# Kernel optimization log

Hardware: AMD Instinct MI355X
Metric: run time of the kernel (lower is better)

Reference implementation:

```python
import jax, jax.numpy as jnp
import numpy as np

STEPS = 10          # points in t_grid -> STEPS-1 RK4 intervals
TRACE_STEPS = 2     # Hutchinson probes per dynamics eval
T_FINAL = 1.0
CLAMP = 100.0


def odefun(t, z, W1, b1, tw1, W2, b2):
    # time-conditioned 2-layer tanh MLP (canonical FFJORD dynamics)
    h = jnp.tanh(z @ W1 + b1 + t * tw1)
    return h @ W2 + b2


def setup_inputs() -> dict:
    key = jax.random.key(0)
    B, D, H = 2048, 512, 1024
    ks = jax.random.split(key, 4)
    s1 = 1.0 / np.sqrt(D)
    s2 = 1.0 / np.sqrt(H)
    return {
        "x": jax.random.normal(ks[0], (B, D), jnp.float32),
        "W1": jax.random.normal(ks[1], (D, H), jnp.float32) * s1,
        "b1": jnp.zeros((H,), jnp.float32),
        "tw1": jax.random.normal(ks[2], (H,), jnp.float32) * 0.1,
        "W2": jax.random.normal(ks[3], (H, D), jnp.float32) * s2,
        "b2": jnp.zeros((D,), jnp.float32),
    }


def reference(x, W1, b1, tw1, W2, b2):
    params = (W1, b1, tw1, W2, b2)
    B, D = x.shape

    def divergence_estimate(t, z, e):
        # torch detaches z before the grad call -> stop_gradient here
        z_sg = jax.lax.stop_gradient(z)
        f, vjp_fn = jax.vjp(lambda zz: odefun(t, zz, *params), z_sg)
        etf = vjp_fn(e)[0]                      # e^T J  (Hutchinson probe)
        return f, jnp.sum(etf * e, axis=-1)     # [B]

    def augmented_dynamics(t, state, key):
        z = state[:, :-1]                        # [B, D]
        div_est = jnp.zeros((B,), state.dtype)
        f_z = None
        for i in range(TRACE_STEPS):             # small fixed loop
            e = jax.random.randint(jax.random.fold_in(key, i), z.shape, 0, 2).astype(z.dtype) * 2.0 - 1.0
            f_z, div = divergence_estimate(t, z, e)
            div_est = div_est + div
        div_est = jnp.clip(div_est / TRACE_STEPS, -CLAMP, CLAMP)
        return jnp.concatenate([f_z, -div_est[:, None]], axis=-1)

    t_grid = jnp.linspace(0.0, T_FINAL, STEPS)
    state0 = jnp.concatenate([x, jnp.zeros((B, 1), x.dtype)], axis=-1)  # [B, D+1]

    def step(carry, t01):
        state, key = carry
        t0, t1 = t01[0], t01[1]
        dt = t1 - t0
        key, k1k, k2k, k3k, k4k = jax.random.split(key, 5)
        # torchdiffeq 'rk4' = Kutta's 3/8-rule variant (rk4_alt_step_func)
        k1 = augmented_dynamics(t0, state, k1k)
        k2 = augmented_dynamics(t0 + dt / 3.0, state + dt * k1 / 3.0, k2k)
        k3 = augmented_dynamics(t0 + dt * 2.0 / 3.0, state + dt * (k2 - k1 / 3.0), k3k)
        k4 = augmented_dynamics(t1, state + dt * (k1 - k2 + k3), k4k)
        state = state + (k1 + 3.0 * (k2 + k3) + k4) * dt * 0.125
        return (state, key), None

    t_pairs = jnp.stack([t_grid[:-1], t_grid[1:]], axis=-1)  # [STEPS-1, 2]
    (state, _), _ = jax.lax.scan(step, (state0, jax.random.key(1234)), t_pairs)

    rep, probsolve = state[:, :-1], state[:, -1]
    logprob = -0.5 * jnp.sum(rep * rep, axis=-1) + probsolve
    return rep, logprob
```

## Files before the change

kernel.cpp:

```cpp
#include <hip/hip_runtime.h>
#include <stdint.h>


#define B_N 2048
#define D_N 512
#define H_N 1024
#define BD (B_N * D_N)

typedef unsigned short u16;
typedef __attribute__((ext_vector_type(8))) short s16x8;
typedef __attribute__((ext_vector_type(4))) float f32x4;

typedef __attribute__((address_space(1))) const uint32_t ga_u32;
typedef __attribute__((address_space(3))) uint32_t ls_u32;

#if __has_builtin(__builtin_amdgcn_alignbit)
#define ROTL32(x, r) __builtin_amdgcn_alignbit((x), (x), 32 - (r))
#else
#define ROTL32(x, r) (((x) << (r)) | ((x) >> (32 - (r))))
#endif

__device__ __forceinline__ float bf2f(u16 u) {
  union { uint32_t u; float f; } c; c.u = ((uint32_t)u) << 16; return c.f;
}
__device__ __forceinline__ u16 f2bf(float f) {
  union { float f; uint32_t u; } c; c.f = f;
  uint32_t r = c.u + 0x7FFFu + ((c.u >> 16) & 1u);
  return (u16)(r >> 16);
}

struct U2 { uint32_t x, y; };

__device__ __forceinline__ U2 tf2x32(uint32_t k0, uint32_t k1, uint32_t x0, uint32_t x1) {
  uint32_t k2 = k0 ^ k1 ^ 0x1BD11BDAu;
#define RND(r) { x0 += x1; x1 = ROTL32(x1, r); x1 ^= x0; }
  x0 += k0; x1 += k1;
  RND(13) RND(15) RND(26) RND(6)
  x0 += k1; x1 += k2 + 1u;
  RND(17) RND(29) RND(16) RND(24)
  x0 += k2; x1 += k0 + 2u;
  RND(13) RND(15) RND(26) RND(6)
  x0 += k0; x1 += k1 + 3u;
  RND(17) RND(29) RND(16) RND(24)
  x0 += k1; x1 += k2 + 4u;
  RND(13) RND(15) RND(26) RND(6)
  x0 += k2; x1 += k0 + 5u;
#undef RND
  U2 r; r.x = x0; r.y = x1; return r;
}

__global__ void k_keysched(uint32_t* __restrict__ ekeys) {
  if (threadIdx.x != 0 || blockIdx.x != 0) return;
  uint32_t kx = 0u, ky = 1234u;
  for (int s = 0; s < 9; ++s) {
    for (int st = 0; st < 4; ++st) {
      U2 kst = tf2x32(kx, ky, 0u, (uint32_t)(st + 1));
      for (int pr = 0; pr < 2; ++pr) {
        U2 fo = tf2x32(kst.x, kst.y, 0u, (uint32_t)pr);
        U2 k2 = tf2x32(fo.x, fo.y, 0u, 1u);
        ekeys[(s * 4 + st) * 4 + pr * 2 + 0] = k2.x;
        ekeys[(s * 4 + st) * 4 + pr * 2 + 1] = k2.y;
      }
    }
    U2 c = tf2x32(kx, ky, 0u, 0u);
    kx = c.x; ky = c.y;
  }
}

__global__ void k_egen(u16* __restrict__ ebf, const uint32_t* __restrict__ keys, int gs) {
  int t = blockIdx.x * 256 + threadIdx.x;
  int stage = gs + (t >> 16), rem = t & 65535;
  int probe = rem >> 15, idx = rem & 32767;
  uint32_t p0 = (uint32_t)idx * 32;
  uint32_t k0 = keys[stage * 4 + probe * 2], k1 = keys[stage * 4 + probe * 2 + 1];
  uint4* dst = (uint4*)(ebf + (size_t)(stage & 3) * (2 * (size_t)BD) + (size_t)probe * BD + (size_t)idx * 32);
#pragma unroll
  for (int g = 0; g < 4; ++g) {
    uint32_t pr[4];
#pragma unroll
    for (int h = 0; h < 4; ++h) {
      uint32_t c0 = p0 + g * 8 + h * 2;
      U2 r0 = tf2x32(k0, k1, 0u, c0);
      U2 r1 = tf2x32(k0, k1, 0u, c0 + 1u);
      pr[h] = (((r0.x ^ r0.y) & 1u) ? 0x3F80u : 0xBF80u) |
              (((r1.x ^ r1.y) & 1u) ? 0x3F800000u : 0xBF800000u);
    }
    uint4 v; v.x = pr[0]; v.y = pr[1]; v.z = pr[2]; v.w = pr[3];
    dst[g] = v;
  }
}

__global__ void k_init(const float* __restrict__ x, float* __restrict__ z, u16* __restrict__ zin,
                       float* __restrict__ lp, float* __restrict__ d0, float* __restrict__ d1) {
  int i = blockIdx.x * 256 + threadIdx.x;
  if (i < BD) { float v = x[i]; z[i] = v; zin[i] = f2bf(v); }
  if (i < B_N) { lp[i] = 0.f; d0[i] = 0.f; d1[i] = 0.f; }
}

__global__ void k_cvtT(const float* __restrict__ src, u16* __restrict__ dst, int R, int C) {
  int i = blockIdx.x * 256 + threadIdx.x;
  if (i >= R * C) return;
  int c = i / R, r = i - c * R;
  dst[i] = f2bf(src[(size_t)r * C + c]);
}
__global__ void k_cvt(const float* __restrict__ src, u16* __restrict__ dst, int n) {
  int i = blockIdx.x * 256 + threadIdx.x;
  if (i < n) dst[i] = f2bf(src[i]);
}

__global__ void k_sentinel(float* __restrict__ out, int n) {
  int i = blockIdx.x * 256 + threadIdx.x;
  if (i < n) out[i] = 12345.0f;
}

__global__ __launch_bounds__(256)
void k_f1(const u16* __restrict__ zin, const u16* __restrict__ e0g, const u16* __restrict__ e1g,
          const u16* __restrict__ W1T, const u16* __restrict__ W2b,
          const float* __restrict__ b1, const float* __restrict__ tw1, float tstage,
          u16* __restrict__ hbuf, float* __restrict__ div0, float* __restrict__ div1) {
  __shared__ u16 S[2][5 * 2048];
  const int tid = threadIdx.x, wave = tid >> 6, lane = tid & 63;
  const int bm = blockIdx.x >> 4;
  const int bh = blockIdx.x & 15;
  const int row0 = bm * 64, col0 = bh * 64;
  const int wm = wave >> 1, wn = wave & 1, r16 = lane & 15, q = lane >> 4;
  const int srow = lane >> 2, scol = (lane & 3) * 8;

  f32x4 az[2][2], au0[2][2], au1[2][2], av0[2][2], av1[2][2];
#pragma unroll
  for (int i = 0; i < 2; ++i)
#pragma unroll
    for (int j = 0; j < 2; ++j) {
      az[i][j] = (f32x4){0,0,0,0}; au0[i][j] = (f32x4){0,0,0,0}; au1[i][j] = (f32x4){0,0,0,0};
      av0[i][j] = (f32x4){0,0,0,0}; av1[i][j] = (f32x4){0,0,0,0};
    }

  const size_t arow = (size_t)(row0 + wave * 16 + srow) * 512 + scol;
  const size_t brow = (size_t)(col0 + wave * 16 + srow) * 512 + scol;
  auto stage = [&](int kt, int buf) {
    u16* b = &S[buf][0];
    __builtin_amdgcn_global_load_lds((ga_u32*)(zin + arow + kt), (ls_u32*)(b + 0    + wave * 512), 16, 0, 0);
    __builtin_amdgcn_global_load_lds((ga_u32*)(e0g + arow + kt), (ls_u32*)(b + 2048 + wave * 512), 16, 0, 0);
    __builtin_amdgcn_global_load_lds((ga_u32*)(e1g + arow + kt), (ls_u32*)(b + 4096 + wave * 512), 16, 0, 0);
    __builtin_amdgcn_global_load_lds((ga_u32*)(W1T + brow + kt), (ls_u32*)(b + 6144 + wave * 512), 16, 0, 0);
    __builtin_amdgcn_global_load_lds((ga_u32*)(W2b + brow + kt), (ls_u32*)(b + 8192 + wave * 512), 16, 0, 0);
  };
  stage(0, 0);
  for (int it = 0; it < 16; ++it) {
    const int buf = it & 1;
    __syncthreads();
    if (it + 1 < 16) stage((it + 1) * 32, buf ^ 1);
    const u16* b = &S[buf][0];
    s16x8 zf[2], e0f[2], e1f[2], w1f[2], w2f[2];
#pragma unroll
    for (int i = 0; i < 2; ++i) {
      const int ao = (wm * 32 + i * 16 + r16) * 32 + q * 8;
      zf[i]  = *(const s16x8*)(b + 0    + ao);
      e0f[i] = *(const s16x8*)(b + 2048 + ao);
      e1f[i] = *(const s16x8*)(b + 4096 + ao);
    }
#pragma unroll
    for (int j = 0; j < 2; ++j) {
      const int bo = (wn * 32 + j * 16 + r16) * 32 + q * 8;
      w1f[j] = *(const s16x8*)(b + 6144 + bo);
      w2f[j] = *(const s16x8*)(b + 8192 + bo);
    }
#pragma unroll
    for (int i = 0; i < 2; ++i)
#pragma unroll
      for (int j = 0; j < 2; ++j) {
        az[i][j]  = __builtin_amdgcn_mfma_f32_16x16x32_bf16(zf[i],  w1f[j], az[i][j],  0, 0, 0);
        au0[i][j] = __builtin_amdgcn_mfma_f32_16x16x32_bf16(e0f[i], w1f[j], au0[i][j], 0, 0, 0);
        au1[i][j] = __builtin_amdgcn_mfma_f32_16x16x32_bf16(e1f[i], w1f[j], au1[i][j], 0, 0, 0);
        av0[i][j] = __builtin_amdgcn_mfma_f32_16x16x32_bf16(e0f[i], w2f[j], av0[i][j], 0, 0, 0);
        av1[i][j] = __builtin_amdgcn_mfma_f32_16x16x32_bf16(e1f[i], w2f[j], av1[i][j], 0, 0, 0);
      }
  }

  float d0s[2][4], d1s[2][4];
#pragma unroll
  for (int i = 0; i < 2; ++i)
#pragma unroll
    for (int r = 0; r < 4; ++r) { d0s[i][r] = 0.f; d1s[i][r] = 0.f; }

#pragma unroll
  for (int j = 0; j < 2; ++j) {
    const int gcol = col0 + wn * 32 + j * 16 + r16;
    const float colb = b1[gcol] + tstage * tw1[gcol];
#pragma unroll
    for (int i = 0; i < 2; ++i) {
      const int rbase = row0 + wm * 32 + i * 16 + q * 4;
#pragma unroll
      for (int r = 0; r < 4; ++r) {
        float hv = tanhf(az[i][j][r] + colb);
        hbuf[(size_t)(rbase + r) * H_N + gcol] = f2bf(hv);
        float s = 1.f - hv * hv;
        d0s[i][r] += s * au0[i][j][r] * av0[i][j][r];
        d1s[i][r] += s * au1[i][j][r] * av1[i][j][r];
      }
    }
  }
#pragma unroll
  for (int i = 0; i < 2; ++i)
#pragma unroll
    for (int r = 0; r < 4; ++r) {
      float a = d0s[i][r], b = d1s[i][r];
#pragma unroll
      for (int m = 1; m < 16; m <<= 1) { a += __shfl_xor(a, m); b += __shfl_xor(b, m); }
      if (r16 == 0) {
        int grow = row0 + wm * 32 + i * 16 + q * 4 + r;
        atomicAdd(&div0[grow], a);
        atomicAdd(&div1[grow], b);
      }
    }
}

template<int ST>
__global__ __launch_bounds__(256)
void k_f3(const u16* __restrict__ hbuf, const u16* __restrict__ W2T, const float* __restrict__ b2,
          float* __restrict__ z, float* __restrict__ ACC, float* __restrict__ T,
          u16* __restrict__ zin, float dt,
          float* __restrict__ lp, float* __restrict__ div0, float* __restrict__ div1, float wdt) {
  __shared__ u16 S[2][2 * 2048];
  const int tid = threadIdx.x, wave = tid >> 6, lane = tid & 63;
  const int bm = blockIdx.x >> 3;
  const int bn = blockIdx.x & 7;
  const int row0 = bm * 64, col0 = bn * 64;
  const int wm = wave >> 1, wn = wave & 1, r16 = lane & 15, q = lane >> 4;
  const int srow = lane >> 2, scol = (lane & 3) * 8;

  if (bn == 0 && tid < 64) {
    int b = row0 + tid;
    float c = 0.5f * (div0[b] + div1[b]);
    c = fminf(fmaxf(c, -100.f), 100.f);
    lp[b] -= wdt * c;
    div0[b] = 0.f; div1[b] = 0.f;
  }

  f32x4 acc[2][2];
#pragma unroll
  for (int i = 0; i < 2; ++i)
#pragma unroll
    for (int j = 0; j < 2; ++j) acc[i][j] = (f32x4){0,0,0,0};

  const size_t arow = (size_t)(row0 + wave * 16 + srow) * 1024 + scol;
  const size_t brow = (size_t)(col0 + wave * 16 + srow) * 1024 + scol;
  auto stage = [&](int kt, int buf) {
    u16* b = &S[buf][0];
    __builtin_amdgcn_global_load_lds((ga_u32*)(hbuf + arow + kt), (ls_u32*)(b + 0    + wave * 512), 16, 0, 0);
    __builtin_amdgcn_global_load_lds((ga_u32*)(W2T  + brow + kt), (ls_u32*)(b + 2048 + wave * 512), 16, 0, 0);
  };
  stage(0, 0);
  for (int it = 0; it < 32; ++it) {
    const int buf = it & 1;
    __syncthreads();
    if (it + 1 < 32) stage((it + 1) * 32, buf ^ 1);
    const u16* b = &S[buf][0];
    s16x8 af[2], bfr[2];
#pragma unroll
    for (int i = 0; i < 2; ++i)
      af[i] = *(const s16x8*)(b + (wm * 32 + i * 16 + r16) * 32 + q * 8);
#pragma unroll
    for (int j = 0; j < 2; ++j)
      bfr[j] = *(const s16x8*)(b + 2048 + (wn * 32 + j * 16 + r16) * 32 + q * 8);
#pragma unroll
    for (int i = 0; i < 2; ++i)
#pragma unroll
      for (int j = 0; j < 2; ++j)
        acc[i][j] = __builtin_amdgcn_mfma_f32_16x16x32_bf16(af[i], bfr[j], acc[i][j], 0, 0, 0);
  }

#pragma unroll
  for (int j = 0; j < 2; ++j) {
    const int gcol = col0 + wn * 32 + j * 16 + r16;
    const float cb = b2[gcol];
#pragma unroll
    for (int i = 0; i < 2; ++i) {
      const int rbase = row0 + wm * 32 + i * 16 + q * 4;
#pragma unroll
      for (int r = 0; r < 4; ++r) {
        const size_t idx = (size_t)(rbase + r) * D_N + gcol;
        const float f = acc[i][j][r] + cb;
        if (ST == 0) {
          ACC[idx] = dt * 0.125f * f;
          T[idx]   = dt * f;
          zin[idx] = f2bf(z[idx] + dt * f * (1.f / 3.f));
        } else if (ST == 1) {
          float t_ = T[idx];
          ACC[idx] += 0.375f * dt * f;
          zin[idx] = f2bf(z[idx] + dt * f - t_ * (1.f / 3.f));
          T[idx]   = t_ - dt * f;
        } else if (ST == 2) {
          ACC[idx] += 0.375f * dt * f;
          zin[idx] = f2bf(z[idx] + T[idx] + dt * f);
        } else {
          float zn = z[idx] + ACC[idx] + dt * 0.125f * f;
          z[idx]   = zn;
          zin[idx] = f2bf(zn);
        }
      }
    }
  }
}

__global__ void k_out(const float* __restrict__ z, const float* __restrict__ lp,
                      float* __restrict__ out) {
  int b = blockIdx.x, t = threadIdx.x;
  const float* zr = z + (size_t)b * D_N;
  float ss = 0.f;
  for (int d = t; d < D_N; d += 256) {
    float v = zr[d];
    out[(size_t)b * D_N + d] = v;
    ss += v * v;
  }
  for (int off = 32; off > 0; off >>= 1) ss += __shfl_down(ss, off);
  __shared__ float red[4];
  if ((t & 63) == 0) red[t >> 6] = ss;
  __syncthreads();
  if (t == 0) out[(size_t)BD + b] = -0.5f * (red[0] + red[1] + red[2] + red[3]) + lp[b];
}

extern "C" void kernel_launch(void* const* d_in, const int* in_sizes, int n_in,
                              void* d_out, int out_size, void* d_ws, size_t ws_size,
                              hipStream_t stream) {
  const float* x   = (const float*)d_in[0];
  const float* W1  = (const float*)d_in[1];
  const float* b1  = (const float*)d_in[2];
  const float* tw1 = (const float*)d_in[3];
  const float* W2  = (const float*)d_in[4];
  const float* b2  = (const float*)d_in[5];

  const size_t NEEDED = (size_t)45 << 20;
  if (ws_size < NEEDED) {
    k_sentinel<<<(BD + B_N + 255) / 256, 256, 0, stream>>>((float*)d_out, BD + B_N);
    return;
  }
  char* w = (char*)d_ws;
  auto carve = [&](size_t bytes) { char* p = w; w += (bytes + 255) & ~(size_t)255; return p; };
  uint32_t* keys = (uint32_t*)carve(144 * sizeof(uint32_t));
  u16* ebf   = (u16*)carve((size_t)4 * 2 * BD * 2);
  float* z   = (float*)carve((size_t)BD * 4);
  float* ACC = (float*)carve((size_t)BD * 4);
  float* T   = (float*)carve((size_t)BD * 4);
  u16* zin   = (u16*)carve((size_t)BD * 2);
  u16* hbuf  = (u16*)carve((size_t)B_N * H_N * 2);
  u16* W1T   = (u16*)carve((size_t)H_N * D_N * 2);
  u16* W2b   = (u16*)carve((size_t)H_N * D_N * 2);
  u16* W2T   = (u16*)carve((size_t)D_N * H_N * 2);
  float* lp   = (float*)carve((size_t)B_N * 4);
  float* div0 = (float*)carve((size_t)B_N * 4);
  float* div1 = (float*)carve((size_t)B_N * 4);

  k_keysched<<<1, 1, 0, stream>>>(keys);
  k_init<<<BD / 256, 256, 0, stream>>>(x, z, zin, lp, div0, div1);
  k_cvtT<<<(D_N * H_N) / 256, 256, 0, stream>>>(W1, W1T, D_N, H_N);
  k_cvt <<<(H_N * D_N) / 256, 256, 0, stream>>>(W2, W2b, H_N * D_N);
  k_cvtT<<<(H_N * D_N) / 256, 256, 0, stream>>>(W2, W2T, H_N, D_N);

  const int gF1 = (B_N / 64) * (H_N / 64);
  const int gF3 = (B_N / 64) * (D_N / 64);

  for (int s = 0; s < 9; ++s) {
    float t0 = (float)s / 9.0f;
    float t1 = (float)(s + 1) / 9.0f;
    float dt = t1 - t0;
    float tst[4] = { t0, t0 + dt / 3.0f, t0 + dt * 2.0f / 3.0f, t1 };
    float wts[4] = { 1.f, 3.f, 3.f, 1.f };
    for (int st = 0; st < 4; ++st) {
      const int sg = s * 4 + st;
      if ((sg & 3) == 0) k_egen<<<1024, 256, 0, stream>>>(ebf, keys, sg);
      const u16* e0g = ebf + (size_t)(sg & 3) * (2 * (size_t)BD);
      const u16* e1g = e0g + BD;
      k_f1<<<gF1, 256, 0, stream>>>(zin, e0g, e1g, W1T, W2b, b1, tw1, tst[st], hbuf, div0, div1);
      const float wdt = dt * 0.125f * wts[st];
      if (st == 0)      k_f3<0><<<gF3, 256, 0, stream>>>(hbuf, W2T, b2, z, ACC, T, zin, dt, lp, div0, div1, wdt);
      else if (st == 1) k_f3<1><<<gF3, 256, 0, stream>>>(hbuf, W2T, b2, z, ACC, T, zin, dt, lp, div0, div1, wdt);
      else if (st == 2) k_f3<2><<<gF3, 256, 0, stream>>>(hbuf, W2T, b2, z, ACC, T, zin, dt, lp, div0, div1, wdt);
      else              k_f3<3><<<gF3, 256, 0, stream>>>(hbuf, W2T, b2, z, ACC, T, zin, dt, lp, div0, div1, wdt);
    }
  }
  k_out<<<B_N, 256, 0, stream>>>(z, lp, (float*)d_out);
}
```

Baseline: 1.476 ms.

## Fuse whole ODE solve into one persistent cooperative kernel with grid syncs

Replaces the per-stage launches of the f1/f3 GEMM kernels with a single cooperative persistent kernel that loops over all 36 RK stages, separated by grid-wide syncs, and folds init, weight conversion and output into it. All Rademacher probes are precomputed up front into a much larger buffer (36 stages instead of 4). The f3 tile is also shrunk to 64x32 so there are 512 tiles, evenly spread across the persistent blocks. This removes launch gaps, at the cost of a larger workspace requirement, grid-sync overhead, and lower per-wave MFMA reuse in f3.

```diff
diff --git a/kernel.cpp b/kernel.cpp
--- a/kernel.cpp
+++ b/kernel.cpp
@@ -1,4 +1,5 @@
 #include <hip/hip_runtime.h>
+#include <hip/hip_cooperative_groups.h>
 #include <stdint.h>
 
 
@@ -6,6 +7,8 @@
 #define D_N 512
 #define H_N 1024
 #define BD (B_N * D_N)
+
+namespace cg = cooperative_groups;
 
 typedef unsigned short u16;
 typedef __attribute__((ext_vector_type(8))) short s16x8;
@@ -20,9 +23,6 @@
 #define ROTL32(x, r) (((x) << (r)) | ((x) >> (32 - (r))))
 #endif
 
-__device__ __forceinline__ float bf2f(u16 u) {
-  union { uint32_t u; float f; } c; c.u = ((uint32_t)u) << 16; return c.f;
-}
 __device__ __forceinline__ u16 f2bf(float f) {
   union { float f; uint32_t u; } c; c.f = f;
   uint32_t r = c.u + 0x7FFFu + ((c.u >> 16) & 1u);
@@ -49,8 +49,7 @@
   U2 r; r.x = x0; r.y = x1; return r;
 }
 
-__global__ void k_keysched(uint32_t* __restrict__ ekeys) {
-  if (threadIdx.x != 0 || blockIdx.x != 0) return;
+__device__ __forceinline__ void keysched_body(uint32_t* ekeys) {
   uint32_t kx = 0u, ky = 1234u;
   for (int s = 0; s < 9; ++s) {
     for (int st = 0; st < 4; ++st) {
@@ -67,13 +66,13 @@
   }
 }
 
-__global__ void k_egen(u16* __restrict__ ebf, const uint32_t* __restrict__ keys, int gs) {
-  int t = blockIdx.x * 256 + threadIdx.x;
-  int stage = gs + (t >> 16), rem = t & 65535;
+__device__ __forceinline__ void egen_item(int t2, u16* __restrict__ ebf,
+                                          const uint32_t* __restrict__ keys) {
+  int stage = t2 >> 16, rem = t2 & 65535;
   int probe = rem >> 15, idx = rem & 32767;
   uint32_t p0 = (uint32_t)idx * 32;
   uint32_t k0 = keys[stage * 4 + probe * 2], k1 = keys[stage * 4 + probe * 2 + 1];
-  uint4* dst = (uint4*)(ebf + (size_t)(stage & 3) * (2 * (size_t)BD) + (size_t)probe * BD + (size_t)idx * 32);
+  uint4* dst = (uint4*)(ebf + (size_t)stage * (2 * (size_t)BD) + (size_t)probe * BD + (size_t)idx * 32);
 #pragma unroll
   for (int g = 0; g < 4; ++g) {
     uint32_t pr[4];
@@ -90,38 +89,13 @@
   }
 }
 
-__global__ void k_init(const float* __restrict__ x, float* __restrict__ z, u16* __restrict__ zin,
-                       float* __restrict__ lp, float* __restrict__ d0, float* __restrict__ d1) {
-  int i = blockIdx.x * 256 + threadIdx.x;
-  if (i < BD) { float v = x[i]; z[i] = v; zin[i] = f2bf(v); }
-  if (i < B_N) { lp[i] = 0.f; d0[i] = 0.f; d1[i] = 0.f; }
-}
-
-__global__ void k_cvtT(const float* __restrict__ src, u16* __restrict__ dst, int R, int C) {
-  int i = blockIdx.x * 256 + threadIdx.x;
-  if (i >= R * C) return;
-  int c = i / R, r = i - c * R;
-  dst[i] = f2bf(src[(size_t)r * C + c]);
-}
-__global__ void k_cvt(const float* __restrict__ src, u16* __restrict__ dst, int n) {
-  int i = blockIdx.x * 256 + threadIdx.x;
-  if (i < n) dst[i] = f2bf(src[i]);
-}
-
-__global__ void k_sentinel(float* __restrict__ out, int n) {
-  int i = blockIdx.x * 256 + threadIdx.x;
-  if (i < n) out[i] = 12345.0f;
-}
-
-__global__ __launch_bounds__(256)
-void k_f1(const u16* __restrict__ zin, const u16* __restrict__ e0g, const u16* __restrict__ e1g,
-          const u16* __restrict__ W1T, const u16* __restrict__ W2b,
-          const float* __restrict__ b1, const float* __restrict__ tw1, float tstage,
-          u16* __restrict__ hbuf, float* __restrict__ div0, float* __restrict__ div1) {
-  __shared__ u16 S[2][5 * 2048];
+__device__ __forceinline__ void f1_tile(u16* S, int tile,
+    const u16* __restrict__ zin, const u16* __restrict__ e0g, const u16* __restrict__ e1g,
+    const u16* __restrict__ W1T, const u16* __restrict__ W2b,
+    const float* __restrict__ b1v, const float* __restrict__ tw1v, float tstage,
+    u16* __restrict__ hbuf, float* __restrict__ div0, float* __restrict__ div1) {
   const int tid = threadIdx.x, wave = tid >> 6, lane = tid & 63;
-  const int bm = blockIdx.x >> 4;
-  const int bh = blockIdx.x & 15;
+  const int bm = tile >> 4, bh = tile & 15;
   const int row0 = bm * 64, col0 = bh * 64;
   const int wm = wave >> 1, wn = wave & 1, r16 = lane & 15, q = lane >> 4;
   const int srow = lane >> 2, scol = (lane & 3) * 8;
@@ -138,7 +112,7 @@
   const size_t arow = (size_t)(row0 + wave * 16 + srow) * 512 + scol;
   const size_t brow = (size_t)(col0 + wave * 16 + srow) * 512 + scol;
   auto stage = [&](int kt, int buf) {
-    u16* b = &S[buf][0];
+    u16* b = S + buf * 10240;
     __builtin_amdgcn_global_load_lds((ga_u32*)(zin + arow + kt), (ls_u32*)(b + 0    + wave * 512), 16, 0, 0);
     __builtin_amdgcn_global_load_lds((ga_u32*)(e0g + arow + kt), (ls_u32*)(b + 2048 + wave * 512), 16, 0, 0);
     __builtin_amdgcn_global_load_lds((ga_u32*)(e1g + arow + kt), (ls_u32*)(b + 4096 + wave * 512), 16, 0, 0);
@@ -150,7 +124,7 @@
     const int buf = it & 1;
     __syncthreads();
     if (it + 1 < 16) stage((it + 1) * 32, buf ^ 1);
-    const u16* b = &S[buf][0];
+    const u16* b = S + buf * 10240;
     s16x8 zf[2], e0f[2], e1f[2], w1f[2], w2f[2];
 #pragma unroll
     for (int i = 0; i < 2; ++i) {
@@ -186,7 +160,7 @@
 #pragma unroll
   for (int j = 0; j < 2; ++j) {
     const int gcol = col0 + wn * 32 + j * 16 + r16;
-    const float colb = b1[gcol] + tstage * tw1[gcol];
+    const float colb = b1v[gcol] + tstage * tw1v[gcol];
 #pragma unroll
     for (int i = 0; i < 2; ++i) {
       const int rbase = row0 + wm * 32 + i * 16 + q * 4;
@@ -204,29 +178,26 @@
   for (int i = 0; i < 2; ++i)
 #pragma unroll
     for (int r = 0; r < 4; ++r) {
-      float a = d0s[i][r], b = d1s[i][r];
-#pragma unroll
-      for (int m = 1; m < 16; m <<= 1) { a += __shfl_xor(a, m); b += __shfl_xor(b, m); }
+      float a = d0s[i][r], bb = d1s[i][r];
+#pragma unroll
+      for (int m = 1; m < 16; m <<= 1) { a += __shfl_xor(a, m); bb += __shfl_xor(bb, m); }
       if (r16 == 0) {
         int grow = row0 + wm * 32 + i * 16 + q * 4 + r;
         atomicAdd(&div0[grow], a);
-        atomicAdd(&div1[grow], b);
+        atomicAdd(&div1[grow], bb);
       }
     }
 }
 
-template<int ST>
-__global__ __launch_bounds__(256)
-void k_f3(const u16* __restrict__ hbuf, const u16* __restrict__ W2T, const float* __restrict__ b2,
-          float* __restrict__ z, float* __restrict__ ACC, float* __restrict__ T,
-          u16* __restrict__ zin, float dt,
-          float* __restrict__ lp, float* __restrict__ div0, float* __restrict__ div1, float wdt) {
-  __shared__ u16 S[2][2 * 2048];
+__device__ __forceinline__ void f3_tile(u16* S, int tile,
+    const u16* __restrict__ hbuf, const u16* __restrict__ W2T, const float* __restrict__ b2v,
+    float* __restrict__ z, float* __restrict__ ACC, float* __restrict__ T,
+    u16* __restrict__ zin, float dt, int st,
+    float* __restrict__ lp, float* __restrict__ div0, float* __restrict__ div1, float wdt) {
   const int tid = threadIdx.x, wave = tid >> 6, lane = tid & 63;
-  const int bm = blockIdx.x >> 3;
-  const int bn = blockIdx.x & 7;
-  const int row0 = bm * 64, col0 = bn * 64;
-  const int wm = wave >> 1, wn = wave & 1, r16 = lane & 15, q = lane >> 4;
+  const int bm = tile >> 4, bn = tile & 15;
+  const int row0 = bm * 64, col0 = bn * 32;
+  const int r16 = lane & 15, q = lane >> 4;
   const int srow = lane >> 2, scol = (lane & 3) * 8;
 
   if (bn == 0 && tid < 64) {
@@ -237,72 +208,167 @@
     div0[b] = 0.f; div1[b] = 0.f;
   }
 
-  f32x4 acc[2][2];
-#pragma unroll
-  for (int i = 0; i < 2; ++i)
-#pragma unroll
-    for (int j = 0; j < 2; ++j) acc[i][j] = (f32x4){0,0,0,0};
+  f32x4 acc[2];
+  acc[0] = (f32x4){0,0,0,0}; acc[1] = (f32x4){0,0,0,0};
 
   const size_t arow = (size_t)(row0 + wave * 16 + srow) * 1024 + scol;
-  const size_t brow = (size_t)(col0 + wave * 16 + srow) * 1024 + scol;
+  const size_t brow = (size_t)(col0 + (wave & 1) * 16 + srow) * 1024 + scol;
   auto stage = [&](int kt, int buf) {
-    u16* b = &S[buf][0];
-    __builtin_amdgcn_global_load_lds((ga_u32*)(hbuf + arow + kt), (ls_u32*)(b + 0    + wave * 512), 16, 0, 0);
-    __builtin_amdgcn_global_load_lds((ga_u32*)(W2T  + brow + kt), (ls_u32*)(b + 2048 + wave * 512), 16, 0, 0);
+    u16* b = S + buf * 10240;
+    __builtin_amdgcn_global_load_lds((ga_u32*)(hbuf + arow + kt), (ls_u32*)(b + wave * 512), 16, 0, 0);
+    if (wave < 2)
+      __builtin_amdgcn_global_load_lds((ga_u32*)(W2T + brow + kt), (ls_u32*)(b + 2048 + wave * 512), 16, 0, 0);
   };
   stage(0, 0);
   for (int it = 0; it < 32; ++it) {
     const int buf = it & 1;
     __syncthreads();
     if (it + 1 < 32) stage((it + 1) * 32, buf ^ 1);
-    const u16* b = &S[buf][0];
-    s16x8 af[2], bfr[2];
-#pragma unroll
-    for (int i = 0; i < 2; ++i)
-      af[i] = *(const s16x8*)(b + (wm * 32 + i * 16 + r16) * 32 + q * 8);
-#pragma unroll
-    for (int j = 0; j < 2; ++j)
-      bfr[j] = *(const s16x8*)(b + 2048 + (wn * 32 + j * 16 + r16) * 32 + q * 8);
-#pragma unroll
-    for (int i = 0; i < 2; ++i)
-#pragma unroll
-      for (int j = 0; j < 2; ++j)
-        acc[i][j] = __builtin_amdgcn_mfma_f32_16x16x32_bf16(af[i], bfr[j], acc[i][j], 0, 0, 0);
+    const u16* b = S + buf * 10240;
+    s16x8 af  = *(const s16x8*)(b + (wave * 16 + r16) * 32 + q * 8);
+    s16x8 bf0 = *(const s16x8*)(b + 2048 + r16 * 32 + q * 8);
+    s16x8 bf1 = *(const s16x8*)(b + 2048 + (16 + r16) * 32 + q * 8);
+    acc[0] = __builtin_amdgcn_mfma_f32_16x16x32_bf16(af, bf0, acc[0], 0, 0, 0);
+    acc[1] = __builtin_amdgcn_mfma_f32_16x16x32_bf16(af, bf1, acc[1], 0, 0, 0);
   }
 
 #pragma unroll
   for (int j = 0; j < 2; ++j) {
-    const int gcol = col0 + wn * 32 + j * 16 + r16;
-    const float cb = b2[gcol];
-#pragma unroll
-    for (int i = 0; i < 2; ++i) {
-      const int rbase = row0 + wm * 32 + i * 16 + q * 4;
-#pragma unroll
-      for (int r = 0; r < 4; ++r) {
-        const size_t idx = (size_t)(rbase + r) * D_N + gcol;
-        const float f = acc[i][j][r] + cb;
-        if (ST == 0) {
-          ACC[idx] = dt * 0.125f * f;
-          T[idx]   = dt * f;
-          zin[idx] = f2bf(z[idx] + dt * f * (1.f / 3.f));
-        } else if (ST == 1) {
-          float t_ = T[idx];
-          ACC[idx] += 0.375f * dt * f;
-          zin[idx] = f2bf(z[idx] + dt * f - t_ * (1.f / 3.f));
-          T[idx]   = t_ - dt * f;
-        } else if (ST == 2) {
-          ACC[idx] += 0.375f * dt * f;
-          zin[idx] = f2bf(z[idx] + T[idx] + dt * f);
-        } else {
-          float zn = z[idx] + ACC[idx] + dt * 0.125f * f;
-          z[idx]   = zn;
-          zin[idx] = f2bf(zn);
-        }
+    const int gcol = col0 + j * 16 + r16;
+    const float cb = b2v[gcol];
+    const int rbase = row0 + wave * 16 + q * 4;
+#pragma unroll
+    for (int r = 0; r < 4; ++r) {
+      const size_t idx = (size_t)(rbase + r) * D_N + gcol;
+      const float f = acc[j][r] + cb;
+      if (st == 0) {
+        ACC[idx] = dt * 0.125f * f;
+        T[idx]   = dt * f;
+        zin[idx] = f2bf(z[idx] + dt * f * (1.f / 3.f));
+      } else if (st == 1) {
+        float t_ = T[idx];
+        ACC[idx] += 0.375f * dt * f;
+        zin[idx] = f2bf(z[idx] + dt * f - t_ * (1.f / 3.f));
+        T[idx]   = t_ - dt * f;
+      } else if (st == 2) {
+        ACC[idx] += 0.375f * dt * f;
+        zin[idx] = f2bf(z[idx] + T[idx] + dt * f);
+      } else {
+        float zn = z[idx] + ACC[idx] + dt * 0.125f * f;
+        z[idx]   = zn;
+        zin[idx] = f2bf(zn);
       }
     }
   }
 }
 
+__global__ __launch_bounds__(256, 2)
+void k_main(const float* __restrict__ x, const float* __restrict__ W1,
+            const float* __restrict__ b1v, const float* __restrict__ tw1v,
+            const float* __restrict__ W2, const float* __restrict__ b2v,
+            float* __restrict__ out, uint32_t* __restrict__ keys, u16* __restrict__ ebf,
+            float* __restrict__ z, float* __restrict__ ACC, float* __restrict__ T,
+            u16* __restrict__ zin, u16* __restrict__ hbuf,
+            u16* __restrict__ W1T, u16* __restrict__ W2b, u16* __restrict__ W2T,
+            float* __restrict__ lp, float* __restrict__ div0, float* __restrict__ div1) {
+  __shared__ u16 S[2 * 10240];
+  cg::grid_group grid = cg::this_grid();
+  const int gtid = blockIdx.x * 256 + threadIdx.x;
+  const int gsz = gridDim.x * 256;
+
+  if (gtid == 0) keysched_body(keys);
+  for (int i = gtid; i < BD; i += gsz) { float v = x[i]; z[i] = v; zin[i] = f2bf(v); }
+  for (int i = gtid; i < B_N; i += gsz) { lp[i] = 0.f; div0[i] = 0.f; div1[i] = 0.f; }
+  for (int i = gtid; i < D_N * H_N; i += gsz) {
+    int c = i / D_N, r = i - c * D_N;
+    W1T[i] = f2bf(W1[(size_t)r * H_N + c]);
+  }
+  for (int i = gtid; i < H_N * D_N; i += gsz) W2b[i] = f2bf(W2[i]);
+  for (int i = gtid; i < H_N * D_N; i += gsz) {
+    int c = i / H_N, r = i - c * H_N;
+    W2T[i] = f2bf(W2[(size_t)r * D_N + c]);
+  }
+  __threadfence();
+  grid.sync();
+
+  for (int t2 = gtid; t2 < 36 * 65536; t2 += gsz) egen_item(t2, ebf, keys);
+  __threadfence();
+  grid.sync();
+
+  for (int sg = 0; sg < 36; ++sg) {
+    const int s = sg >> 2, st = sg & 3;
+    const float t0 = (float)s / 9.0f, t1 = (float)(s + 1) / 9.0f, dt = t1 - t0;
+    const float tst = (st == 0) ? t0 : (st == 1) ? (t0 + dt / 3.0f)
+                   : (st == 2) ? (t0 + dt * 2.0f / 3.0f) : t1;
+    const float wdt = dt * 0.125f * ((st == 1 || st == 2) ? 3.0f : 1.0f);
+    const u16* e0g = ebf + (size_t)sg * (2 * (size_t)BD);
+    const u16* e1g = e0g + BD;
+    for (int tile = blockIdx.x; tile < 512; tile += gridDim.x)
+      f1_tile(S, tile, zin, e0g, e1g, W1T, W2b, b1v, tw1v, tst, hbuf, div0, div1);
+    __threadfence();
+    grid.sync();
+    for (int tile = blockIdx.x; tile < 512; tile += gridDim.x)
+      f3_tile(S, tile, hbuf, W2T, b2v, z, ACC, T, zin, dt, st, lp, div0, div1, wdt);
+    __threadfence();
+    grid.sync();
+  }
+
+  const int wave = threadIdx.x >> 6, lane = threadIdx.x & 63;
+  for (int rb = blockIdx.x; rb < 512; rb += gridDim.x) {
+    int b = rb * 4 + wave;
+    const float* zr = z + (size_t)b * D_N;
+    float ss = 0.f;
+    for (int d = lane; d < D_N; d += 64) {
+      float v = zr[d];
+      out[(size_t)b * D_N + d] = v;
+      ss += v * v;
+    }
+    for (int off = 32; off; off >>= 1) ss += __shfl_down(ss, off);
+    if (lane == 0) out[BD + b] = -0.5f * ss + lp[b];
+  }
+}
+
+__global__ void k_keysched(uint32_t* __restrict__ ekeys) {
+  if (threadIdx.x == 0 && blockIdx.x == 0) keysched_body(ekeys);
+}
+__global__ void kegen_g(u16* __restrict__ ebf, const uint32_t* __restrict__ keys) {
+  int t = blockIdx.x * 256 + threadIdx.x;
+  if (t < 36 * 65536) egen_item(t, ebf, keys);
+}
+__global__ void k_init(const float* __restrict__ x, float* __restrict__ z, u16* __restrict__ zin,
+                       float* __restrict__ lp, float* __restrict__ d0, float* __restrict__ d1) {
+  int i = blockIdx.x * 256 + threadIdx.x;
+  if (i < BD) { float v = x[i]; z[i] = v; zin[i] = f2bf(v); }
+  if (i < B_N) { lp[i] = 0.f; d0[i] = 0.f; d1[i] = 0.f; }
+}
+__global__ void k_cvtT(const float* __restrict__ src, u16* __restrict__ dst, int R, int C) {
+  int i = blockIdx.x * 256 + threadIdx.x;
+  if (i >= R * C) return;
+  int c = i / R, r = i - c * R;
+  dst[i] = f2bf(src[(size_t)r * C + c]);
+}
+__global__ void k_cvt(const float* __restrict__ src, u16* __restrict__ dst, int n) {
+  int i = blockIdx.x * 256 + threadIdx.x;
+  if (i < n) dst[i] = f2bf(src[i]);
+}
+__global__ void k_sentinel(float* __restrict__ out, int n) {
+  int i = blockIdx.x * 256 + threadIdx.x;
+  if (i < n) out[i] = 12345.0f;
+}
+__global__ __launch_bounds__(256) void kf1_g(
+    const u16* zin, const u16* e0g, const u16* e1g, const u16* W1T, const u16* W2b,
+    const float* b1v, const float* tw1v, float tstage,
+    u16* hbuf, float* div0, float* div1) {
+  __shared__ u16 S[2 * 10240];
+  f1_tile(S, blockIdx.x, zin, e0g, e1g, W1T, W2b, b1v, tw1v, tstage, hbuf, div0, div1);
+}
+__global__ __launch_bounds__(256) void kf3_g(
+    const u16* hbuf, const u16* W2T, const float* b2v,
+    float* z, float* ACC, float* T, u16* zin, float dt, int st,
+    float* lp, float* div0, float* div1, float wdt) {
+  __shared__ u16 S[2 * 10240];
+  f3_tile(S, blockIdx.x, hbuf, W2T, b2v, z, ACC, T, zin, dt, st, lp, div0, div1, wdt);
+}
 __global__ void k_out(const float* __restrict__ z, const float* __restrict__ lp,
                       float* __restrict__ out) {
   int b = blockIdx.x, t = threadIdx.x;
@@ -329,16 +395,17 @@
   const float* tw1 = (const float*)d_in[3];
   const float* W2  = (const float*)d_in[4];
   const float* b2  = (const float*)d_in[5];
-
-  const size_t NEEDED = (size_t)45 << 20;
+  float* outp = (float*)d_out;
+
+  const size_t NEEDED = (size_t)180 << 20;
   if (ws_size < NEEDED) {
-    k_sentinel<<<(BD + B_N + 255) / 256, 256, 0, stream>>>((float*)d_out, BD + B_N);
+    k_sentinel<<<(BD + B_N + 255) / 256, 256, 0, stream>>>(outp, BD + B_N);
     return;
   }
   char* w = (char*)d_ws;
   auto carve = [&](size_t bytes) { char* p = w; w += (bytes + 255) & ~(size_t)255; return p; };
   uint32_t* keys = (uint32_t*)carve(144 * sizeof(uint32_t));
-  u16* ebf   = (u16*)carve((size_t)4 * 2 * BD * 2);
+  u16* ebf   = (u16*)carve((size_t)36 * 2 * BD * 2);
   float* z   = (float*)carve((size_t)BD * 4);
   float* ACC = (float*)carve((size_t)BD * 4);
   float* T   = (float*)carve((size_t)BD * 4);
@@ -351,14 +418,27 @@
   float* div0 = (float*)carve((size_t)B_N * 4);
   float* div1 = (float*)carve((size_t)B_N * 4);
 
+  int maxb = 0;
+  hipError_t orc = hipOccupancyMaxActiveBlocksPerMultiprocessor(&maxb, (const void*)k_main, 256, 0);
+  if (orc == hipSuccess && maxb >= 1) {
+    int nb = maxb * 256;
+    if (nb > 512) nb = 512;
+    void* params[] = { (void*)&x, (void*)&W1, (void*)&b1, (void*)&tw1, (void*)&W2, (void*)&b2,
+                       (void*)&outp, (void*)&keys, (void*)&ebf, (void*)&z, (void*)&ACC, (void*)&T,
+                       (void*)&zin, (void*)&hbuf, (void*)&W1T, (void*)&W2b, (void*)&W2T,
+                       (void*)&lp, (void*)&div0, (void*)&div1 };
+    hipError_t rc = hipLaunchCooperativeKernel((const void*)k_main, dim3(nb), dim3(256),
+                                               params, 0, stream);
+    if (rc == hipSuccess) return;
+    (void)hipGetLastError();
+  }
+
   k_keysched<<<1, 1, 0, stream>>>(keys);
   k_init<<<BD / 256, 256, 0, stream>>>(x, z, zin, lp, div0, div1);
   k_cvtT<<<(D_N * H_N) / 256, 256, 0, stream>>>(W1, W1T, D_N, H_N);
   k_cvt <<<(H_N * D_N) / 256, 256, 0, stream>>>(W2, W2b, H_N * D_N);
   k_cvtT<<<(H_N * D_N) / 256, 256, 0, stream>>>(W2, W2T, H_N, D_N);
-
-  const int gF1 = (B_N / 64) * (H_N / 64);
-  const int gF3 = (B_N / 64) * (D_N / 64);
+  kegen_g<<<(36 * 65536) / 256, 256, 0, stream>>>(ebf, keys);
 
   for (int s = 0; s < 9; ++s) {
     float t0 = (float)s / 9.0f;
@@ -368,16 +448,12 @@
     float wts[4] = { 1.f, 3.f, 3.f, 1.f };
     for (int st = 0; st < 4; ++st) {
       const int sg = s * 4 + st;
-      if ((sg & 3) == 0) k_egen<<<1024, 256, 0, stream>>>(ebf, keys, sg);
-      const u16* e0g = ebf + (size_t)(sg & 3) * (2 * (size_t)BD);
+      const u16* e0g = ebf + (size_t)sg * (2 * (size_t)BD);
       const u16* e1g = e0g + BD;
-      k_f1<<<gF1, 256, 0, stream>>>(zin, e0g, e1g, W1T, W2b, b1, tw1, tst[st], hbuf, div0, div1);
-      const float wdt = dt * 0.125f * wts[st];
-      if (st == 0)      k_f3<0><<<gF3, 256, 0, stream>>>(hbuf, W2T, b2, z, ACC, T, zin, dt, lp, div0, div1, wdt);
-      else if (st == 1) k_f3<1><<<gF3, 256, 0, stream>>>(hbuf, W2T, b2, z, ACC, T, zin, dt, lp, div0, div1, wdt);
-      else if (st == 2) k_f3<2><<<gF3, 256, 0, stream>>>(hbuf, W2T, b2, z, ACC, T, zin, dt, lp, div0, div1, wdt);
-      else              k_f3<3><<<gF3, 256, 0, stream>>>(hbuf, W2T, b2, z, ACC, T, zin, dt, lp, div0, div1, wdt);
-    }
-  }
-  k_out<<<B_N, 256, 0, stream>>>(z, lp, (float*)d_out);
-}
+      kf1_g<<<512, 256, 0, stream>>>(zin, e0g, e1g, W1T, W2b, b1, tw1, tst[st], hbuf, div0, div1);
+      kf3_g<<<512, 256, 0, stream>>>(hbuf, W2T, b2, z, ACC, T, zin, dt, st,
+                                     lp, div0, div1, dt * 0.125f * wts[st]);
+    }
+  }
+  k_out<<<B_N, 256, 0, stream>>>(z, lp, outp);
+}
```

After: 5.658 ms. 3.83x slower.
